# Kernel tuning notes

Measured on AMD Instinct MI355X. Metric: run time of the kernel, lower is better.

The kernel has to match this reference:

```python
import jax, jax.numpy as jnp
import numpy as np

# db4 decomposition low-pass filter (pywt convention, 8 taps)
DEC_LO = np.array([-0.010597401784997278, 0.032883011666982945, 0.030841381835986965,
                   -0.18703481171888114, -0.02798376941698385, 0.6308807679295904,
                   0.7148465705525415, 0.23037781330885523], dtype=np.float32)
L = DEC_LO.shape[0]  # 8
REC_LO = DEC_LO[::-1].copy()
DEC_HI = (REC_LO * ((-1.0) ** (np.arange(L) + 1))).astype(np.float32)
REC_HI = DEC_HI[::-1].copy()
LEVEL = 7

# lax.conv does correlation; flip filters to get true convolution (pywt semantics)
K_DEC = jnp.asarray(np.stack([DEC_LO[::-1], DEC_HI[::-1]])[:, None, :])  # [2,1,L] out-ch: (lo, hi)
K_REC = jnp.asarray(np.stack([REC_LO[::-1], REC_HI[::-1]])[None, :, :])  # [1,2,L] in-ch: (ca, cd)


def dwt(x):
    # x: [B, N]. pywt zero-mode dwt == full conv then take odd indices;
    # fused here as stride-2 conv with asymmetric padding (L-2, L-1).
    y = jax.lax.conv_general_dilated(x[:, None, :], K_DEC, (2,), [(L - 2, L - 1)])
    return y[:, 0], y[:, 1]  # each [B, floor((N+L-1)/2)]


def idwt(ca, cd):
    # upsample-by-2 (lhs_dilation, length 2n-1), full conv, trim L-2 each side -> pad (1,1)
    y = jax.lax.conv_general_dilated(jnp.stack([ca, cd], axis=1), K_REC, (1,),
                                     [(1, 1)], lhs_dilation=(2,))
    return y[:, 0]  # [B, 2n - L + 2]


def soft(c, t):
    # pywt.threshold(mode='soft')
    return jnp.sign(c) * jnp.maximum(jnp.abs(c) - t, 0.0)


def setup_inputs() -> dict:
    key = jax.random.key(0)
    k1, k2 = jax.random.split(key)
    x = jax.random.normal(k1, (32768, 1116), dtype=jnp.float32)
    # learned scalar parameter, initialized like nn.Parameter(torch.tensor(0.02))
    raw_threshold = jnp.asarray(0.02, dtype=jnp.float32)
    return {"x": x, "raw_threshold": raw_threshold}


def reference(x, raw_threshold):
    thr = jnp.maximum(raw_threshold, 0.01)  # torch.clamp(min=0.01)
    # wavedec: 7-level analysis
    a = x
    details = []
    for _ in range(LEVEL):
        a, d = dwt(a)
        details.append(d)
    # soft-threshold every coefficient band (including approximation)
    a = soft(a, thr)
    details = [soft(d, thr) for d in details]
    # waverec: synthesis, truncating cA when one sample longer than cD (pywt rule)
    for d in reversed(details):
        if a.shape[-1] > d.shape[-1]:
            a = a[:, : d.shape[-1]]
        a = idwt(a, d)
    return a  # [B, 1116]
```

## Files before the change

### kernel.cpp

```cpp
#include <hip/hip_runtime.h>

#define NCOL 1116
#define NLEV 7
#define NT 256
#define RPB 4
#define ARENA 2048

static __device__ __forceinline__ float softf(float c, float t) {
    float m = fabsf(c) - t;
    return m > 0.0f ? copysignf(m, c) : 0.0f;
}

__global__ __launch_bounds__(NT)
void wavelet_kernel(const float* __restrict__ x,
                    const float* __restrict__ thr_ptr,
                    float* __restrict__ out, int nrow) {
    constexpr float DEC_LO[8] = {-0.010597401784997278f,  0.032883011666982945f,
                                  0.030841381835986965f, -0.18703481171888114f,
                                 -0.02798376941698385f,   0.6308807679295904f,
                                  0.7148465705525415f,    0.23037781330885523f};
    constexpr float DEC_HI[8] = {-0.23037781330885523f,   0.7148465705525415f,
                                 -0.6308807679295904f,   -0.02798376941698385f,
                                  0.18703481171888114f,   0.030841381835986965f,
                                 -0.032883011666982945f, -0.010597401784997278f};
    constexpr float REC_LO[8] = { 0.23037781330885523f,   0.7148465705525415f,
                                  0.6308807679295904f,   -0.02798376941698385f,
                                 -0.18703481171888114f,   0.030841381835986965f,
                                  0.032883011666982945f, -0.010597401784997278f};
    constexpr float REC_HI[8] = {-0.010597401784997278f, -0.032883011666982945f,
                                  0.030841381835986965f,  0.18703481171888114f,
                                 -0.02798376941698385f,  -0.6308807679295904f,
                                  0.7148465705525415f,   -0.23037781330885523f};

    constexpr int alen[8] = {1116, 561, 284, 145, 76, 41, 24, 15};
    constexpr int doff[7] = {8, 570, 854, 1000, 1076, 2008, 2032};

    __shared__ __align__(16) float SH[RPB * ARENA];

    const int lane = threadIdx.x & 63;
    const int wv   = threadIdx.x >> 6;
    const int row  = blockIdx.x * RPB + wv;
    if (row >= nrow) return;

    const float thr = fmaxf(thr_ptr[0], 0.01f);

    float* const arena = SH + wv * ARENA;
    float* const a8 = arena + 8;
    float* const b8 = arena + 1140;
    float* const c8 = arena + 1716;

    {
        const float4* xr = (const float4*)(x + (size_t)row * NCOL);
        float4* dst = (float4*)a8;
        for (int i = lane; i < NCOL / 4; i += 64) dst[i] = xr[i];
        if (lane < 14) { int j = lane < 6 ? lane - 6 : 1110 + lane; a8[j] = 0.0f; }
    }
    __builtin_amdgcn_wave_barrier();

    {
        float* cur = a8;
        float* nxt = b8;
        #pragma unroll
        for (int l = 0; l < NLEV; ++l) {
            const int nout = alen[l + 1];
            float* dp = arena + doff[l];
            for (int b = lane; 2 * b < nout; b += 64) {
                const int o = 2 * b;
                const float* src = cur + o + o - 6;
                float v[10];
                #pragma unroll
                for (int j = 0; j < 10; ++j) v[j] = src[j];
                float lo0 = 0.f, hi0 = 0.f, lo1 = 0.f, hi1 = 0.f;
                #pragma unroll
                for (int s = 0; s < 8; ++s) {
                    lo0 = fmaf(DEC_LO[s], v[7 - s], lo0);
                    hi0 = fmaf(DEC_HI[s], v[7 - s], hi0);
                    lo1 = fmaf(DEC_LO[s], v[9 - s], lo1);
                    hi1 = fmaf(DEC_HI[s], v[9 - s], hi1);
                }
                float av0 = (l == NLEV - 1) ? softf(lo0, thr) : lo0;
                float dv0 = softf(hi0, thr);
                if (o + 1 < nout) {
                    float av1 = (l == NLEV - 1) ? softf(lo1, thr) : lo1;
                    *(float2*)(nxt + o) = make_float2(av0, av1);
                    *(float2*)(dp + o)  = make_float2(dv0, softf(hi1, thr));
                } else {
                    nxt[o] = av0;
                    dp[o]  = dv0;
                }
            }
            if (l < NLEV - 1) {
                if (lane < 15) {
                    int j = lane < 6 ? lane - 6 : nout + lane - 6;
                    nxt[j] = 0.0f;
                }
            }
            __builtin_amdgcn_wave_barrier();
            if (l == 0) { cur = b8; nxt = c8; }
            else       { float* t = cur; cur = nxt; nxt = t; }
        }
    }

    {
        float* cur = b8;
        float* nxt = c8;
        #pragma unroll
        for (int l = NLEV - 1; l >= 1; --l) {
            const int M = alen[l + 1];
            const float* dp = arena + doff[l];
            const int npair = M - 3;
            for (int b = lane; 2 * b < npair; b += 64) {
                const int m = 2 * b;
                float ca[5], cd[5];
                #pragma unroll
                for (int j = 0; j < 5; ++j) { ca[j] = cur[m + j]; cd[j] = dp[m + j]; }
                float y0 = fmaf(REC_LO[0], ca[3], fmaf(REC_LO[2], ca[2], fmaf(REC_LO[4], ca[1], REC_LO[6] * ca[0])));
                y0 = fmaf(REC_HI[0], cd[3], fmaf(REC_HI[2], cd[2], fmaf(REC_HI[4], cd[1], fmaf(REC_HI[6], cd[0], y0))));
                float y1 = fmaf(REC_LO[1], ca[3], fmaf(REC_LO[3], ca[2], fmaf(REC_LO[5], ca[1], REC_LO[7] * ca[0])));
                y1 = fmaf(REC_HI[1], cd[3], fmaf(REC_HI[3], cd[2], fmaf(REC_HI[5], cd[1], fmaf(REC_HI[7], cd[0], y1))));
                if (m + 1 < npair) {
                    float y2 = fmaf(REC_LO[0], ca[4], fmaf(REC_LO[2], ca[3], fmaf(REC_LO[4], ca[2], REC_LO[6] * ca[1])));
                    y2 = fmaf(REC_HI[0], cd[4], fmaf(REC_HI[2], cd[3], fmaf(REC_HI[4], cd[2], fmaf(REC_HI[6], cd[1], y2))));
                    float y3 = fmaf(REC_LO[1], ca[4], fmaf(REC_LO[3], ca[3], fmaf(REC_LO[5], ca[2], REC_LO[7] * ca[1])));
                    y3 = fmaf(REC_HI[1], cd[4], fmaf(REC_HI[3], cd[3], fmaf(REC_HI[5], cd[2], fmaf(REC_HI[7], cd[1], y3))));
                    *(float4*)(nxt + 2 * m) = make_float4(y0, y1, y2, y3);
                } else {
                    nxt[2 * m]     = y0;
                    nxt[2 * m + 1] = y1;
                }
            }
            __builtin_amdgcn_wave_barrier();
            float* t = cur; cur = nxt; nxt = t;
        }
        {
            const float* dp = arena + doff[0];
            float4* orow = (float4*)(out + (size_t)row * NCOL);
            const int npair = alen[1] - 3;
            for (int b = lane; 2 * b < npair; b += 64) {
                const int m = 2 * b;
                float ca[5], cd[5];
                #pragma unroll
                for (int j = 0; j < 5; ++j) { ca[j] = cur[m + j]; cd[j] = dp[m + j]; }
                float y0 = fmaf(REC_LO[0], ca[3], fmaf(REC_LO[2], ca[2], fmaf(REC_LO[4], ca[1], REC_LO[6] * ca[0])));
                y0 = fmaf(REC_HI[0], cd[3], fmaf(REC_HI[2], cd[2], fmaf(REC_HI[4], cd[1], fmaf(REC_HI[6], cd[0], y0))));
                float y1 = fmaf(REC_LO[1], ca[3], fmaf(REC_LO[3], ca[2], fmaf(REC_LO[5], ca[1], REC_LO[7] * ca[0])));
                y1 = fmaf(REC_HI[1], cd[3], fmaf(REC_HI[3], cd[2], fmaf(REC_HI[5], cd[1], fmaf(REC_HI[7], cd[0], y1))));
                float y2 = fmaf(REC_LO[0], ca[4], fmaf(REC_LO[2], ca[3], fmaf(REC_LO[4], ca[2], REC_LO[6] * ca[1])));
                y2 = fmaf(REC_HI[0], cd[4], fmaf(REC_HI[2], cd[3], fmaf(REC_HI[4], cd[2], fmaf(REC_HI[6], cd[1], y2))));
                float y3 = fmaf(REC_LO[1], ca[4], fmaf(REC_LO[3], ca[3], fmaf(REC_LO[5], ca[2], REC_LO[7] * ca[1])));
                y3 = fmaf(REC_HI[1], cd[4], fmaf(REC_HI[3], cd[3], fmaf(REC_HI[5], cd[2], fmaf(REC_HI[7], cd[1], y3))));
                orow[b] = make_float4(y0, y1, y2, y3);
            }
        }
    }
}

extern "C" void kernel_launch(void* const* d_in, const int* in_sizes, int n_in,
                              void* d_out, int out_size, void* d_ws, size_t ws_size,
                              hipStream_t stream) {
    const float* x = (const float*)d_in[0];
    const float* thr = (const float*)d_in[1];
    float* out = (float*)d_out;
    const int nrow = in_sizes[0] / NCOL;
    const int nblk = (nrow + RPB - 1) / RPB;
    hipLaunchKernelGGL(wavelet_kernel, dim3(nblk), dim3(NT), 0, stream, x, thr, out, nrow);
}
```

Baseline: 273.3 us.

## Compute first DWT level directly from global memory and restructure level loops

The first analysis level now reads the input row straight from global memory with float2 loads, handling the edges with bounds checks, instead of staging the whole row in LDS first. This removes the row copy and the LDS space it took, so the detail arena is repacked and the buffers shifted. Each lane now computes one output per step instead of two, and the loops are fully unrolled with compile-time trip counts. The soft threshold is rewritten in branchless form. The cost is more global-load instructions with uncoalesced stride-2 float2 access and less reuse of overlapping filter windows per thread.

```diff
diff --git a/kernel.cpp b/kernel.cpp
--- a/kernel.cpp
+++ b/kernel.cpp
@@ -7,8 +7,7 @@
 #define ARENA 2048
 
 static __device__ __forceinline__ float softf(float c, float t) {
-    float m = fabsf(c) - t;
-    return m > 0.0f ? copysignf(m, c) : 0.0f;
+    return copysignf(fmaxf(fabsf(c) - t, 0.0f), c);
 }
 
 __global__ __launch_bounds__(NT)
@@ -33,7 +32,7 @@
                                   0.7148465705525415f,   -0.23037781330885523f};
 
     constexpr int alen[8] = {1116, 561, 284, 145, 76, 41, 24, 15};
-    constexpr int doff[7] = {8, 570, 854, 1000, 1076, 2008, 2032};
+    constexpr int doff[7] = {0, 562, 846, 992, 1068, 1110, 1134};
 
     __shared__ __align__(16) float SH[RPB * ARENA];
 
@@ -45,72 +44,88 @@
     const float thr = fmaxf(thr_ptr[0], 0.01f);
 
     float* const arena = SH + wv * ARENA;
-    float* const a8 = arena + 8;
-    float* const b8 = arena + 1140;
-    float* const c8 = arena + 1716;
+    float* const dpool = arena;
+    float* const b8    = arena + 1156;
+    float* const c8    = arena + 1732;
 
     {
-        const float4* xr = (const float4*)(x + (size_t)row * NCOL);
-        float4* dst = (float4*)a8;
-        for (int i = lane; i < NCOL / 4; i += 64) dst[i] = xr[i];
-        if (lane < 14) { int j = lane < 6 ? lane - 6 : 1110 + lane; a8[j] = 0.0f; }
-    }
-    __builtin_amdgcn_wave_barrier();
-
-    {
-        float* cur = a8;
-        float* nxt = b8;
+        const float* xrow = x + (size_t)row * NCOL;
         #pragma unroll
-        for (int l = 0; l < NLEV; ++l) {
-            const int nout = alen[l + 1];
-            float* dp = arena + doff[l];
-            for (int b = lane; 2 * b < nout; b += 64) {
-                const int o = 2 * b;
-                const float* src = cur + o + o - 6;
-                float v[10];
-                #pragma unroll
-                for (int j = 0; j < 10; ++j) v[j] = src[j];
-                float lo0 = 0.f, hi0 = 0.f, lo1 = 0.f, hi1 = 0.f;
+        for (int k = 0; k < 9; ++k) {
+            const int o = lane + (k << 6);
+            if (o < 561) {
+                float v[8];
+                if (o >= 3 && o <= 557) {
+                    const float2* p = (const float2*)(xrow + 2 * o - 6);
+                    float2 q0 = p[0], q1 = p[1], q2 = p[2], q3 = p[3];
+                    v[0] = q0.x; v[1] = q0.y; v[2] = q1.x; v[3] = q1.y;
+                    v[4] = q2.x; v[5] = q2.y; v[6] = q3.x; v[7] = q3.y;
+                } else {
+                    #pragma unroll
+                    for (int j = 0; j < 8; ++j) {
+                        const int idx = 2 * o - 6 + j;
+                        v[j] = (idx >= 0 && idx < NCOL) ? xrow[idx] : 0.0f;
+                    }
+                }
+                float lo = 0.0f, hi = 0.0f;
                 #pragma unroll
                 for (int s = 0; s < 8; ++s) {
-                    lo0 = fmaf(DEC_LO[s], v[7 - s], lo0);
-                    hi0 = fmaf(DEC_HI[s], v[7 - s], hi0);
-                    lo1 = fmaf(DEC_LO[s], v[9 - s], lo1);
-                    hi1 = fmaf(DEC_HI[s], v[9 - s], hi1);
+                    lo = fmaf(DEC_LO[s], v[7 - s], lo);
+                    hi = fmaf(DEC_HI[s], v[7 - s], hi);
                 }
-                float av0 = (l == NLEV - 1) ? softf(lo0, thr) : lo0;
-                float dv0 = softf(hi0, thr);
-                if (o + 1 < nout) {
-                    float av1 = (l == NLEV - 1) ? softf(lo1, thr) : lo1;
-                    *(float2*)(nxt + o) = make_float2(av0, av1);
-                    *(float2*)(dp + o)  = make_float2(dv0, softf(hi1, thr));
-                } else {
-                    nxt[o] = av0;
-                    dp[o]  = dv0;
-                }
+                b8[o]    = lo;
+                dpool[o] = softf(hi, thr);
             }
-            if (l < NLEV - 1) {
-                if (lane < 15) {
-                    int j = lane < 6 ? lane - 6 : nout + lane - 6;
-                    nxt[j] = 0.0f;
-                }
-            }
-            __builtin_amdgcn_wave_barrier();
-            if (l == 0) { cur = b8; nxt = c8; }
-            else       { float* t = cur; cur = nxt; nxt = t; }
         }
+        if (lane < 14) { const int j = lane < 6 ? lane - 6 : 555 + lane; b8[j] = 0.0f; }
+        __builtin_amdgcn_wave_barrier();
     }
 
-    {
-        float* cur = b8;
-        float* nxt = c8;
+    #pragma unroll
+    for (int l = 1; l < NLEV; ++l) {
+        const int nout = alen[l + 1];
+        float* const cur = (l & 1) ? b8 : c8;
+        float* const nxt = (l & 1) ? c8 : b8;
+        float* const dp  = dpool + doff[l];
+        const int K = (nout + 63) >> 6;
         #pragma unroll
-        for (int l = NLEV - 1; l >= 1; --l) {
-            const int M = alen[l + 1];
-            const float* dp = arena + doff[l];
-            const int npair = M - 3;
-            for (int b = lane; 2 * b < npair; b += 64) {
-                const int m = 2 * b;
+        for (int k = 0; k < K; ++k) {
+            const int o = lane + (k << 6);
+            if (o < nout) {
+                const float2* p = (const float2*)(cur + 2 * o - 6);
+                float2 q0 = p[0], q1 = p[1], q2 = p[2], q3 = p[3];
+                float v[8];
+                v[0] = q0.x; v[1] = q0.y; v[2] = q1.x; v[3] = q1.y;
+                v[4] = q2.x; v[5] = q2.y; v[6] = q3.x; v[7] = q3.y;
+                float lo = 0.0f, hi = 0.0f;
+                #pragma unroll
+                for (int s = 0; s < 8; ++s) {
+                    lo = fmaf(DEC_LO[s], v[7 - s], lo);
+                    hi = fmaf(DEC_HI[s], v[7 - s], hi);
+                }
+                nxt[o] = (l == NLEV - 1) ? softf(lo, thr) : lo;
+                dp[o]  = softf(hi, thr);
+            }
+        }
+        if (l < NLEV - 1 && lane < 14) {
+            const int j = lane < 6 ? lane - 6 : nout + lane - 6;
+            nxt[j] = 0.0f;
+        }
+        __builtin_amdgcn_wave_barrier();
+    }
+
+    #pragma unroll
+    for (int l = NLEV - 1; l >= 1; --l) {
+        const int M = alen[l + 1];
+        const int npair = M - 3;
+        const float* const cur = (l & 1) ? c8 : b8;
+        float* const nxt       = (l & 1) ? b8 : c8;
+        const float* const dp  = dpool + doff[l];
+        const int KI = (((npair + 1) >> 1) + 63) >> 6;
+        #pragma unroll
+        for (int kk = 0; kk < KI; ++kk) {
+            const int m = (lane + (kk << 6)) << 1;
+            if (m < npair) {
                 float ca[5], cd[5];
                 #pragma unroll
                 for (int j = 0; j < 5; ++j) { ca[j] = cur[m + j]; cd[j] = dp[m + j]; }
@@ -129,15 +144,19 @@
                     nxt[2 * m + 1] = y1;
                 }
             }
-            __builtin_amdgcn_wave_barrier();
-            float* t = cur; cur = nxt; nxt = t;
         }
-        {
-            const float* dp = arena + doff[0];
-            float4* orow = (float4*)(out + (size_t)row * NCOL);
-            const int npair = alen[1] - 3;
-            for (int b = lane; 2 * b < npair; b += 64) {
-                const int m = 2 * b;
+        __builtin_amdgcn_wave_barrier();
+    }
+
+    {
+        const float* const cur = b8;
+        const float* const dp  = dpool;
+        float4* orow = (float4*)(out + (size_t)row * NCOL);
+        #pragma unroll
+        for (int kk = 0; kk < 5; ++kk) {
+            const int bq = lane + (kk << 6);
+            const int m = bq << 1;
+            if (m < 558) {
                 float ca[5], cd[5];
                 #pragma unroll
                 for (int j = 0; j < 5; ++j) { ca[j] = cur[m + j]; cd[j] = dp[m + j]; }
@@ -149,7 +168,7 @@
                 y2 = fmaf(REC_HI[0], cd[4], fmaf(REC_HI[2], cd[3], fmaf(REC_HI[4], cd[2], fmaf(REC_HI[6], cd[1], y2))));
                 float y3 = fmaf(REC_LO[1], ca[4], fmaf(REC_LO[3], ca[3], fmaf(REC_LO[5], ca[2], REC_LO[7] * ca[1])));
                 y3 = fmaf(REC_HI[1], cd[4], fmaf(REC_HI[3], cd[3], fmaf(REC_HI[5], cd[2], fmaf(REC_HI[7], cd[1], y3))));
-                orow[b] = make_float4(y0, y1, y2, y3);
+                orow[bq] = make_float4(y0, y1, y2, y3);
             }
         }
     }
```

Result: faster. 254.3 us (-7.0%).
